# Kernel tuning notes

Measured on AMD Instinct MI355X. Metric: run time of the kernel, lower is better.

Reference implementation:

```python
import jax, jax.numpy as jnp
import numpy as np


def _conv1x1(t, W, b):
    # 1x1 conv == per-pixel channel GEMM: [B,C,H,W] x [O,C] -> [B,O,H,W]
    return jnp.einsum('bchw,oc->bohw', t, W) + b[None, :, None, None]


def setup_inputs() -> dict:
    key = jax.random.key(0)
    ks = jax.random.split(key, 10)
    B, C, H, W = 8, 256, 96, 96
    s = 1.0 / np.sqrt(C)
    inp = {
        'x': jax.random.normal(ks[0], (B, C, H, W), dtype=jnp.float32),
        'Wq': jax.random.normal(ks[1], (C, C), dtype=jnp.float32) * s,
        'bq': jax.random.normal(ks[2], (C,), dtype=jnp.float32) * 0.01,
        'Wk': jax.random.normal(ks[3], (C, C), dtype=jnp.float32) * s,
        'bk': jax.random.normal(ks[4], (C,), dtype=jnp.float32) * 0.01,
        'Wv': jax.random.normal(ks[5], (C, C), dtype=jnp.float32) * s,
        'bv': jax.random.normal(ks[6], (C,), dtype=jnp.float32) * 0.01,
        'Ws': jax.random.normal(ks[7], (C, C), dtype=jnp.float32) * s,
        'bs': jax.random.normal(ks[8], (C,), dtype=jnp.float32) * 0.01,
        # torch init is zeros; use a nonzero scalar so the attention branch matters
        'gamma': jax.random.normal(ks[9], (1,), dtype=jnp.float32) * 0.5,
    }
    return inp


def reference(x, Wq, bq, Wk, bk, Wv, bv, Ws, bs, gamma):
    B, C, H, W = x.shape
    N = H * W
    # query: [B, N, C]
    q = _conv1x1(x, Wq, bq).reshape(B, C, N).transpose(0, 2, 1)
    # key: 1x1 conv, then stride-3 1x1 conv (== subsample every 3rd pixel, then GEMM)
    k = _conv1x1(x, Wk, bk)
    k = _conv1x1(k[:, :, ::3, ::3], Ws, bs)
    Ns = k.shape[2] * k.shape[3]
    k = k.reshape(B, C, Ns)
    energy = jnp.einsum('bnc,bcm->bnm', q, k)       # [B, N, Ns]
    attn = jax.nn.softmax(energy, axis=-1)
    # value: same 1x1 conv + strided 1x1 conv pipeline
    v = _conv1x1(x, Wv, bv)
    v = _conv1x1(v[:, :, ::3, ::3], Ws, bs).reshape(B, C, Ns)
    out = jnp.einsum('bcm,bnm->bcn', v, attn).reshape(B, C, H, W)
    return gamma[0] * out + x
```

## Files before the change

kernel.cpp:

```cpp
#include <hip/hip_runtime.h>

typedef _Float16 f16;
typedef _Float16 f16x8 __attribute__((ext_vector_type(8)));
typedef __fp16 fp16x2 __attribute__((ext_vector_type(2)));
typedef float f32x4 __attribute__((ext_vector_type(4)));
typedef float f32x16 __attribute__((ext_vector_type(16)));

#define CDIM 256
#define NPIX 9216
#define NB 8

__device__ __forceinline__ f32x4 mfma16(f16x8 a, f16x8 b, f32x4 c) {
  return __builtin_amdgcn_mfma_f32_16x16x32_f16(a, b, c, 0, 0, 0);
}
__device__ __forceinline__ f32x16 mfma32(f16x8 a, f16x8 b, f32x16 c) {
  return __builtin_amdgcn_mfma_f32_32x32x16_f16(a, b, c, 0, 0, 0);
}
__device__ __forceinline__ f16x8 ld8(const f16* p) { return *(const f16x8*)p; }

__device__ __forceinline__ void stage16(const void* g, void* l) {
  __builtin_amdgcn_global_load_lds((const __attribute__((address_space(1))) unsigned int*)g,
                                   (__attribute__((address_space(3))) unsigned int*)l, 16, 0, 0);
}
#define S_BARRIER() do { asm volatile("" ::: "memory"); __builtin_amdgcn_s_barrier(); asm volatile("" ::: "memory"); } while (0)
#define WAIT_VM(N) do { asm volatile("s_waitcnt vmcnt(" #N ")" ::: "memory"); __builtin_amdgcn_sched_barrier(0); } while (0)

__device__ __forceinline__ unsigned pkrtz(float a, float b) {
  union { fp16x2 h; unsigned u; } cv;
  cv.h = __builtin_amdgcn_cvt_pkrtz(a, b);
  return cv.u;
}
union U8 { f16x8 v; unsigned u[4]; };

__device__ __forceinline__ f16x8 pack_swap(float v0, float v1, float v2, float v3,
                                           float v4, float v5, float v6, float v7,
                                           int hh) {
  unsigned a  = pkrtz(v0, v1);
  unsigned b2 = pkrtz(v2, v3);
  unsigned c2 = pkrtz(v4, v5);
  unsigned d2 = pkrtz(v6, v7);
  unsigned ex1 = __shfl_xor(hh ? a : c2, 32);
  unsigned ex2 = __shfl_xor(hh ? b2 : d2, 32);
  U8 r;
  r.u[0] = hh ? ex1 : a;
  r.u[1] = hh ? ex2 : b2;
  r.u[2] = hh ? c2 : ex1;
  r.u[3] = hh ? d2 : ex2;
  return r.v;
}


__global__ void prep_weights(const float* __restrict__ Wq,
                             const float* __restrict__ Wk, const float* __restrict__ bk,
                             const float* __restrict__ Wv, const float* __restrict__ bv,
                             const float* __restrict__ Ws, const float* __restrict__ bs,
                             f16* __restrict__ WqF, f16* __restrict__ Wk2H, f16* __restrict__ Wv2H,
                             float* __restrict__ bk2, float* __restrict__ bv2) {
  int o = blockIdx.x, c = threadIdx.x;
  float ak = 0.f, av = 0.f;
  for (int i = 0; i < CDIM; ++i) {
    float w = Ws[o*CDIM + i];
    ak += w * Wk[i*CDIM + c];
    av += w * Wv[i*CDIM + c];
  }
  Wk2H[o*CDIM + c] = (f16)ak;
  Wv2H[o*CDIM + c] = (f16)av;
  {
    size_t byte = (size_t)((o >> 5)*16 + (c >> 4))*1024
                + (size_t)(((c >> 3) & 1)*32 + (o & 31))*16 + (c & 7)*2;
    *(f16*)((char*)WqF + byte) = (f16)Wq[o*CDIM + c];
  }
  if (c == 0) {
    float sk = 0.f, sv = 0.f;
    for (int i = 0; i < CDIM; ++i) { float w = Ws[o*CDIM + i]; sk += w*bk[i]; sv += w*bv[i]; }
    bk2[o] = sk + bs[o];
    bv2[o] = sv + bs[o];
  }
}

__global__ void transpose_x(const float* __restrict__ x, char* __restrict__ xT) {
  __shared__ f16 tile[32][34];
  int c0 = blockIdx.x * 32, n0 = blockIdx.y * 32, b = blockIdx.z;
  int tx = threadIdx.x, ty = threadIdx.y;
#pragma unroll
  for (int j = 0; j < 4; ++j) {
    int cl = ty + 8*j;
    tile[cl][tx] = (f16)x[(size_t)(b*CDIM + c0 + cl)*NPIX + n0 + tx];
  }
  __syncthreads();
  int tid = ty*32 + tx;
  if (tid < 128) {
    int nl = tid >> 2, u = tid & 3;
    int n = n0 + nl;
    int cu = (c0 >> 3) + u;
    f16x8 v;
#pragma unroll
    for (int e = 0; e < 8; ++e) v[e] = tile[8*u + e][nl];
    size_t byte = (size_t)(b*NPIX + n)*512 + (size_t)((cu ^ (n & 7)) << 4);
    *(f16x8*)(xT + byte) = v;
  }
}

__global__ __launch_bounds__(256) void compute_kv(
    const char* __restrict__ xT, const f16* __restrict__ Wk2H, const f16* __restrict__ Wv2H,
    const float* __restrict__ bk2, const float* __restrict__ bv2,
    char* __restrict__ kB, char* __restrict__ vB) {
  int ch = blockIdx.x;
  int m0 = ch * 32;
  int b = blockIdx.y;
  int tid = threadIdx.x;
  int w = tid >> 6, lane = tid & 63, l15 = lane & 15, q = lane >> 4;
  size_t chbase = (size_t)(b*32 + ch)*16384;

  const char* xrow[2]; int xn7[2];
#pragma unroll
  for (int mt2 = 0; mt2 < 2; ++mt2) {
    int m = m0 + 16*mt2 + l15;
    int n = 288*(m >> 5) + 3*(m & 31);
    xrow[mt2] = xT + (size_t)(b*NPIX + n)*512;
    xn7[mt2] = n & 7;
  }
  const f16 *kwb[4], *vwb[4];
#pragma unroll
  for (int t = 0; t < 4; ++t) {
    kwb[t] = Wk2H + (size_t)(64*w + 16*t + l15)*CDIM + 8*q;
    vwb[t] = Wv2H + (size_t)(64*w + 16*t + l15)*CDIM + 8*q;
  }
  f32x4 accK[2][4] = {};
  f32x4 accV[4][2] = {};
  for (int ks = 0; ks < 8; ++ks) {
    f16x8 am[2], wk[4], wv[4];
#pragma unroll
    for (int mt2 = 0; mt2 < 2; ++mt2)
      am[mt2] = *(const f16x8*)(xrow[mt2] + (((q + 4*ks) ^ xn7[mt2]) << 4));
#pragma unroll
    for (int t = 0; t < 4; ++t) { wk[t] = ld8(kwb[t] + 32*ks); wv[t] = ld8(vwb[t] + 32*ks); }
#pragma unroll
    for (int mt2 = 0; mt2 < 2; ++mt2)
#pragma unroll
      for (int ot = 0; ot < 4; ++ot) {
        accK[mt2][ot] = mfma16(am[mt2], wk[ot], accK[mt2][ot]);
        accV[ot][mt2] = mfma16(wv[ot], am[mt2], accV[ot][mt2]);
      }
  }
#pragma unroll
  for (int mt2 = 0; mt2 < 2; ++mt2)
#pragma unroll
    for (int ot = 0; ot < 4; ++ot) {
      int cin = 64*w + 16*ot + l15;
      float bo = bk2[cin];
      size_t fb = chbase + (size_t)(cin >> 4)*1024 + (size_t)(((cin >> 3) & 1)*32)*16 + (cin & 7)*2;
#pragma unroll
      for (int r = 0; r < 4; ++r) {
        int keyrel = 16*mt2 + 4*q + r;
        *(f16*)(kB + fb + (size_t)keyrel*16) = (f16)(accK[mt2][ot][r] + bo);
      }
    }
#pragma unroll
  for (int ct = 0; ct < 4; ++ct) {
    f32x4 bv4 = *(const f32x4*)(bv2 + 64*w + 16*ct + 4*q);
#pragma unroll
    for (int mt2 = 0; mt2 < 2; ++mt2) {
#pragma unroll
      for (int r = 0; r < 4; ++r) {
        int c = 64*w + 16*ct + 4*q + r;
        size_t byte = chbase + (size_t)(2*(c >> 5) + mt2)*1024
                    + (size_t)((l15 >> 3)*32 + (c & 31))*16 + (l15 & 7)*2;
        *(f16*)(vB + byte) = (f16)(accV[ct][mt2][r] + bv4[r]);
      }
    }
  }
}

__global__ __launch_bounds__(256, 2) void attention(
    const char* __restrict__ xT, const f16* __restrict__ WqF, const float* __restrict__ bq,
    const char* __restrict__ kB, const char* __restrict__ vB,
    const float* __restrict__ xg, const float* __restrict__ gamma_p,
    float* __restrict__ out) {
  __shared__ char lds[65536];

  int bid = blockIdx.x;
  int b = bid & 7;
  int tile = bid >> 3;
  int tid = threadIdx.x;
  int w = tid >> 6, lane = tid & 63, l31 = lane & 31, hh = lane >> 5;
  int n0w = tile*128 + w*32;
  int lane16 = lane * 16;

  const char* kBb = kB + (size_t)b*524288;
  const char* vBb = vB + (size_t)b*524288;

  {
    int so = tid * 16;
#pragma unroll
    for (int r = 0; r < 4; ++r) stage16(kBb + so + r*4096, lds + so + r*4096);
#pragma unroll
    for (int r = 0; r < 4; ++r) stage16(vBb + so + r*4096, lds + 16384 + so + r*4096);
  }

  f16x8 qf[16];
  {
    f16x8 xb[16];
    int n = n0w + l31;
    const char* xrow = xT + (size_t)(b*NPIX + n)*512;
    int n7 = n & 7;
#pragma unroll
    for (int s = 0; s < 16; ++s)
      xb[s] = *(const f16x8*)(xrow + (((2*s + hh) ^ n7) << 4));
#pragma unroll
    for (int ot = 0; ot < 8; ++ot) {
      f32x16 acc;
#pragma unroll
      for (int j = 0; j < 16; ++j) acc[j] = 0.f;
#pragma unroll
      for (int s = 0; s < 16; ++s) {
        f16x8 wa = *(const f16x8*)((const char*)WqF + (size_t)(ot*16 + s)*1024 + lane16);
        acc = mfma32(wa, xb[s], acc);
      }
#pragma unroll
      for (int i = 0; i < 4; ++i) {
        f32x4 bv4 = *(const f32x4*)(bq + 32*ot + 8*i + 4*hh);
#pragma unroll
        for (int j2 = 0; j2 < 4; ++j2) acc[4*i + j2] += bv4[j2];
      }
      qf[2*ot + 0] = pack_swap(acc[0], acc[1], acc[2], acc[3],
                               acc[4], acc[5], acc[6], acc[7], hh);
      qf[2*ot + 1] = pack_swap(acc[8], acc[9], acc[10], acc[11],
                               acc[12], acc[13], acc[14], acc[15], hh);
    }
  }

  f32x16 O[8];
#pragma unroll
  for (int i = 0; i < 8; ++i)
#pragma unroll
    for (int j = 0; j < 16; ++j) O[i][j] = 0.f;
  float m_run = -3e38f, l_run = 0.f;

  for (int t = 0; t < 32; ++t) {
    char* curb = lds + ((t & 1) << 15);
    if (t < 31) {
      const char* ksrc = kBb + (size_t)(t + 1)*16384;
      const char* vsrc = vBb + (size_t)(t + 1)*16384;
      char* kd = lds + (((t + 1) & 1) << 15);
      int so = tid * 16;
#pragma unroll
      for (int r = 0; r < 4; ++r) stage16(ksrc + so + r*4096, kd + so + r*4096);
#pragma unroll
      for (int r = 0; r < 4; ++r) stage16(vsrc + so + r*4096, kd + 16384 + so + r*4096);
      WAIT_VM(8);
    } else {
      WAIT_VM(0);
    }
    S_BARRIER();

    f32x16 S16;
#pragma unroll
    for (int j = 0; j < 16; ++j) S16[j] = 0.f;
    __builtin_amdgcn_s_setprio(1);
#pragma unroll
    for (int s = 0; s < 16; ++s) {
      f16x8 kf = *(const f16x8*)(curb + s*1024 + lane16);
      S16 = mfma32(kf, qf[s], S16);
    }
    __builtin_amdgcn_s_setprio(0);

    float mx = S16[0];
#pragma unroll
    for (int j = 1; j < 16; ++j) mx = fmaxf(mx, S16[j]);
    mx = fmaxf(mx, __shfl_xor(mx, 32));
    if (!__all(mx <= m_run + 8.0f)) {
      float mn = fmaxf(m_run, mx);
      float al = __expf(m_run - mn);
      m_run = mn;
      l_run *= al;
#pragma unroll
      for (int i = 0; i < 8; ++i)
#pragma unroll
        for (int j = 0; j < 16; ++j) O[i][j] *= al;
    }
    float p[16];
    float ls = 0.f;
#pragma unroll
    for (int j = 0; j < 16; ++j) { p[j] = __expf(S16[j] - m_run); ls += p[j]; }
    l_run += ls;

    f16x8 pf0 = pack_swap(p[0], p[1], p[2], p[3], p[4], p[5], p[6], p[7], hh);
    f16x8 pf1 = pack_swap(p[8], p[9], p[10], p[11], p[12], p[13], p[14], p[15], hh);

    __builtin_amdgcn_s_setprio(1);
#pragma unroll
    for (int ct = 0; ct < 8; ++ct) {
      f16x8 vf0 = *(const f16x8*)(curb + 16384 + (ct*2 + 0)*1024 + lane16);
      O[ct] = mfma32(vf0, pf0, O[ct]);
      f16x8 vf1 = *(const f16x8*)(curb + 16384 + (ct*2 + 1)*1024 + lane16);
      O[ct] = mfma32(vf1, pf1, O[ct]);
    }
    __builtin_amdgcn_s_setprio(0);
    S_BARRIER();
  }

  l_run += __shfl_xor(l_run, 32);
  float inv = 1.0f / l_run;
  float g = gamma_p[0];
  int n = n0w + l31;
#pragma unroll
  for (int ct = 0; ct < 8; ++ct)
#pragma unroll
    for (int j = 0; j < 16; ++j) {
      int c = 32*ct + (j & 3) + 8*(j >> 2) + 4*hh;
      size_t idx = (size_t)(b*CDIM + c)*NPIX + n;
      out[idx] = g * (O[ct][j] * inv) + xg[idx];
    }
}

extern "C" void kernel_launch(void* const* d_in, const int* in_sizes, int n_in,
                              void* d_out, int out_size, void* d_ws, size_t ws_size,
                              hipStream_t stream) {
  (void)in_sizes; (void)n_in; (void)out_size; (void)ws_size;
  const float* x     = (const float*)d_in[0];
  const float* Wq    = (const float*)d_in[1];
  const float* bq    = (const float*)d_in[2];
  const float* Wk    = (const float*)d_in[3];
  const float* bk    = (const float*)d_in[4];
  const float* Wv    = (const float*)d_in[5];
  const float* bv    = (const float*)d_in[6];
  const float* Ws    = (const float*)d_in[7];
  const float* bs    = (const float*)d_in[8];
  const float* gamma = (const float*)d_in[9];

  char* ws = (char*)d_ws;
  float* bk2 = (float*)(ws);
  float* bv2 = (float*)(ws + 1024);
  char* xT   = ws + 4096;
  char* kB   = ws + 4096 + 37748736;
  char* vB   = kB + 4194304;
  f16* WqF   = (f16*)(vB + 4194304);
  f16* Wk2H  = WqF + 65536;
  f16* Wv2H  = Wk2H + 65536;

  prep_weights<<<256, 256, 0, stream>>>(Wq, Wk, bk, Wv, bv, Ws, bs, WqF, Wk2H, Wv2H, bk2, bv2);
  transpose_x<<<dim3(8, 288, 8), dim3(32, 8), 0, stream>>>(x, xT);
  compute_kv<<<dim3(32, 8), 256, 0, stream>>>(xT, Wk2H, Wv2H, bk2, bv2, kB, vB);
  attention<<<576, 256, 0, stream>>>(xT, WqF, bq, kB, vB, x, gamma, (float*)d_out);
}
```

Before: 197.2 us.

## Split attention output channels across two wave groups with 512-thread blocks

The attention kernel now runs 8 waves per block. Each pair of waves shares the same 32 query rows and computes the full QK^T and softmax redundantly, but each wave owns only half of the 256 output channels in the PV product. This halves the O accumulator registers per wave and spreads the K/V staging loads over twice as many threads. The QK^T chain is also split into two independent accumulators to shorten the MFMA dependency chain. The cost is that QK^T, the Q projection and the exp work are duplicated in both waves of a pair.

```diff
diff --git a/kernel.cpp b/kernel.cpp
--- a/kernel.cpp
+++ b/kernel.cpp
@@ -172,7 +172,7 @@
   }
 }
 
-__global__ __launch_bounds__(256, 2) void attention(
+__global__ __launch_bounds__(512, 2) void attention(
     const char* __restrict__ xT, const f16* __restrict__ WqF, const float* __restrict__ bq,
     const char* __restrict__ kB, const char* __restrict__ vB,
     const float* __restrict__ xg, const float* __restrict__ gamma_p,
@@ -184,7 +184,8 @@
   int tile = bid >> 3;
   int tid = threadIdx.x;
   int w = tid >> 6, lane = tid & 63, l31 = lane & 31, hh = lane >> 5;
-  int n0w = tile*128 + w*32;
+  int rt = w & 3, cs = w >> 2;
+  int n0w = tile*128 + rt*32;
   int lane16 = lane * 16;
 
   const char* kBb = kB + (size_t)b*524288;
@@ -192,10 +193,10 @@
 
   {
     int so = tid * 16;
-#pragma unroll
-    for (int r = 0; r < 4; ++r) stage16(kBb + so + r*4096, lds + so + r*4096);
-#pragma unroll
-    for (int r = 0; r < 4; ++r) stage16(vBb + so + r*4096, lds + 16384 + so + r*4096);
+    stage16(kBb + so, lds + so);
+    stage16(kBb + so + 8192, lds + so + 8192);
+    stage16(vBb + so, lds + 16384 + so);
+    stage16(vBb + so + 8192, lds + 16384 + so + 8192);
   }
 
   f16x8 qf[16];
@@ -230,9 +231,9 @@
     }
   }
 
-  f32x16 O[8];
-#pragma unroll
-  for (int i = 0; i < 8; ++i)
+  f32x16 O[4];
+#pragma unroll
+  for (int i = 0; i < 4; ++i)
 #pragma unroll
     for (int j = 0; j < 16; ++j) O[i][j] = 0.f;
   float m_run = -3e38f, l_run = 0.f;
@@ -244,26 +245,31 @@
       const char* vsrc = vBb + (size_t)(t + 1)*16384;
       char* kd = lds + (((t + 1) & 1) << 15);
       int so = tid * 16;
-#pragma unroll
-      for (int r = 0; r < 4; ++r) stage16(ksrc + so + r*4096, kd + so + r*4096);
-#pragma unroll
-      for (int r = 0; r < 4; ++r) stage16(vsrc + so + r*4096, kd + 16384 + so + r*4096);
-      WAIT_VM(8);
+      stage16(ksrc + so, kd + so);
+      stage16(ksrc + so + 8192, kd + so + 8192);
+      stage16(vsrc + so, kd + 16384 + so);
+      stage16(vsrc + so + 8192, kd + 16384 + so + 8192);
+      WAIT_VM(4);
     } else {
       WAIT_VM(0);
     }
     S_BARRIER();
 
+    f32x16 Sa, Sb;
+#pragma unroll
+    for (int j = 0; j < 16; ++j) { Sa[j] = 0.f; Sb[j] = 0.f; }
+    __builtin_amdgcn_s_setprio(1);
+#pragma unroll
+    for (int s = 0; s < 8; ++s) {
+      f16x8 kfa = *(const f16x8*)(curb + (2*s)*1024 + lane16);
+      Sa = mfma32(kfa, qf[2*s], Sa);
+      f16x8 kfb = *(const f16x8*)(curb + (2*s + 1)*1024 + lane16);
+      Sb = mfma32(kfb, qf[2*s + 1], Sb);
+    }
+    __builtin_amdgcn_s_setprio(0);
     f32x16 S16;
 #pragma unroll
-    for (int j = 0; j < 16; ++j) S16[j] = 0.f;
-    __builtin_amdgcn_s_setprio(1);
-#pragma unroll
-    for (int s = 0; s < 16; ++s) {
-      f16x8 kf = *(const f16x8*)(curb + s*1024 + lane16);
-      S16 = mfma32(kf, qf[s], S16);
-    }
-    __builtin_amdgcn_s_setprio(0);
+    for (int j = 0; j < 16; ++j) S16[j] = Sa[j] + Sb[j];
 
     float mx = S16[0];
 #pragma unroll
@@ -275,7 +281,7 @@
       m_run = mn;
       l_run *= al;
 #pragma unroll
-      for (int i = 0; i < 8; ++i)
+      for (int i = 0; i < 4; ++i)
 #pragma unroll
         for (int j = 0; j < 16; ++j) O[i][j] *= al;
     }
@@ -290,10 +296,11 @@
 
     __builtin_amdgcn_s_setprio(1);
 #pragma unroll
-    for (int ct = 0; ct < 8; ++ct) {
-      f16x8 vf0 = *(const f16x8*)(curb + 16384 + (ct*2 + 0)*1024 + lane16);
+    for (int ct = 0; ct < 4; ++ct) {
+      int ctg = cs*4 + ct;
+      f16x8 vf0 = *(const f16x8*)(curb + 16384 + (ctg*2 + 0)*1024 + lane16);
       O[ct] = mfma32(vf0, pf0, O[ct]);
-      f16x8 vf1 = *(const f16x8*)(curb + 16384 + (ct*2 + 1)*1024 + lane16);
+      f16x8 vf1 = *(const f16x8*)(curb + 16384 + (ctg*2 + 1)*1024 + lane16);
       O[ct] = mfma32(vf1, pf1, O[ct]);
     }
     __builtin_amdgcn_s_setprio(0);
@@ -305,10 +312,10 @@
   float g = gamma_p[0];
   int n = n0w + l31;
 #pragma unroll
-  for (int ct = 0; ct < 8; ++ct)
+  for (int ct = 0; ct < 4; ++ct)
 #pragma unroll
     for (int j = 0; j < 16; ++j) {
-      int c = 32*ct + (j & 3) + 8*(j >> 2) + 4*hh;
+      int c = 32*(cs*4 + ct) + (j & 3) + 8*(j >> 2) + 4*hh;
       size_t idx = (size_t)(b*CDIM + c)*NPIX + n;
       out[idx] = g * (O[ct][j] * inv) + xg[idx];
     }
@@ -342,5 +349,5 @@
   prep_weights<<<256, 256, 0, stream>>>(Wq, Wk, bk, Wv, bv, Ws, bs, WqF, Wk2H, Wv2H, bk2, bv2);
   transpose_x<<<dim3(8, 288, 8), dim3(32, 8), 0, stream>>>(x, xT);
   compute_kv<<<dim3(32, 8), 256, 0, stream>>>(xT, Wk2H, Wv2H, bk2, bv2, kB, vB);
-  attention<<<576, 256, 0, stream>>>(xT, WqF, bq, kB, vB, x, gamma, (float*)d_out);
-}
+  attention<<<576, 512, 0, stream>>>(xT, WqF, bq, kB, vB, x, gamma, (float*)d_out);
+}
```

After: 269.6 us. 1.37x slower.

## Software-pipeline QK^T one tile ahead with triple-buffered K/V in LDS

Applied to the files above, without the earlier changes.

The attention loop now computes the next tile's QK^T scores while running softmax and PV on the current tile, using two ping-pong score accumulators. K is prefetched two tiles ahead and V one tile ahead into triple-buffered LDS regions (96KB), and the trailing per-iteration barrier and setprio hints are removed. The goal is to overlap exp and softmax VALU work with MFMA and to hide load latency. In exchange, the larger LDS footprint and extra registers drop occupancy from 2 to 1 block per CU.

```diff
diff --git a/kernel.cpp b/kernel.cpp
--- a/kernel.cpp
+++ b/kernel.cpp
@@ -172,12 +172,12 @@
   }
 }
 
-__global__ __launch_bounds__(256, 2) void attention(
+__global__ __launch_bounds__(256, 1) void attention(
     const char* __restrict__ xT, const f16* __restrict__ WqF, const float* __restrict__ bq,
     const char* __restrict__ kB, const char* __restrict__ vB,
     const float* __restrict__ xg, const float* __restrict__ gamma_p,
     float* __restrict__ out) {
-  __shared__ char lds[65536];
+  __shared__ char lds[98304];
 
   int bid = blockIdx.x;
   int b = bid & 7;
@@ -189,13 +189,16 @@
 
   const char* kBb = kB + (size_t)b*524288;
   const char* vBb = vB + (size_t)b*524288;
+  char* vbase = lds + 49152;
 
   {
     int so = tid * 16;
 #pragma unroll
     for (int r = 0; r < 4; ++r) stage16(kBb + so + r*4096, lds + so + r*4096);
 #pragma unroll
-    for (int r = 0; r < 4; ++r) stage16(vBb + so + r*4096, lds + 16384 + so + r*4096);
+    for (int r = 0; r < 4; ++r) stage16(vBb + so + r*4096, vbase + so + r*4096);
+#pragma unroll
+    for (int r = 0; r < 4; ++r) stage16(kBb + 16384 + so + r*4096, lds + 16384 + so + r*4096);
   }
 
   f16x8 qf[16];
@@ -229,6 +232,8 @@
                                acc[12], acc[13], acc[14], acc[15], hh);
     }
   }
+  WAIT_VM(0);
+  S_BARRIER();
 
   f32x16 O[8];
 #pragma unroll
@@ -236,38 +241,48 @@
 #pragma unroll
     for (int j = 0; j < 16; ++j) O[i][j] = 0.f;
   float m_run = -3e38f, l_run = 0.f;
-
-  for (int t = 0; t < 32; ++t) {
-    char* curb = lds + ((t & 1) << 15);
+  float g = gamma_p[0];
+
+  f32x16 SA, SB;
+#pragma unroll
+  for (int j = 0; j < 16; ++j) SA[j] = 0.f;
+#pragma unroll
+  for (int s = 0; s < 16; ++s) {
+    f16x8 kf = *(const f16x8*)(lds + s*1024 + lane16);
+    SA = mfma32(kf, qf[s], SA);
+  }
+
+  auto body = [&](f32x16& Scur, f32x16& Snext, int t) {
+    int so = tid * 16;
+    if (t + 2 < 32) {
+      const char* ksrc = kBb + (size_t)(t + 2)*16384;
+      char* kd = lds + ((t + 2) % 3)*16384;
+#pragma unroll
+      for (int r = 0; r < 4; ++r) stage16(ksrc + so + r*4096, kd + so + r*4096);
+    }
+    if (t + 1 < 32) {
+      const char* vsrc = vBb + (size_t)(t + 1)*16384;
+      char* vd = vbase + ((t + 1) % 3)*16384;
+#pragma unroll
+      for (int r = 0; r < 4; ++r) stage16(vsrc + so + r*4096, vd + so + r*4096);
+    }
+    if (t < 30) { WAIT_VM(8); } else if (t == 30) { WAIT_VM(4); } else { WAIT_VM(0); }
+    S_BARRIER();
+
     if (t < 31) {
-      const char* ksrc = kBb + (size_t)(t + 1)*16384;
-      const char* vsrc = vBb + (size_t)(t + 1)*16384;
-      char* kd = lds + (((t + 1) & 1) << 15);
-      int so = tid * 16;
-#pragma unroll
-      for (int r = 0; r < 4; ++r) stage16(ksrc + so + r*4096, kd + so + r*4096);
-#pragma unroll
-      for (int r = 0; r < 4; ++r) stage16(vsrc + so + r*4096, kd + 16384 + so + r*4096);
-      WAIT_VM(8);
-    } else {
-      WAIT_VM(0);
-    }
-    S_BARRIER();
-
-    f32x16 S16;
-#pragma unroll
-    for (int j = 0; j < 16; ++j) S16[j] = 0.f;
-    __builtin_amdgcn_s_setprio(1);
-#pragma unroll
-    for (int s = 0; s < 16; ++s) {
-      f16x8 kf = *(const f16x8*)(curb + s*1024 + lane16);
-      S16 = mfma32(kf, qf[s], S16);
-    }
-    __builtin_amdgcn_s_setprio(0);
-
-    float mx = S16[0];
-#pragma unroll
-    for (int j = 1; j < 16; ++j) mx = fmaxf(mx, S16[j]);
+      const char* kc = lds + ((t + 1) % 3)*16384;
+#pragma unroll
+      for (int j = 0; j < 16; ++j) Snext[j] = 0.f;
+#pragma unroll
+      for (int s = 0; s < 16; ++s) {
+        f16x8 kf = *(const f16x8*)(kc + s*1024 + lane16);
+        Snext = mfma32(kf, qf[s], Snext);
+      }
+    }
+
+    float mx = Scur[0];
+#pragma unroll
+    for (int j = 1; j < 16; ++j) mx = fmaxf(mx, Scur[j]);
     mx = fmaxf(mx, __shfl_xor(mx, 32));
     if (!__all(mx <= m_run + 8.0f)) {
       float mn = fmaxf(m_run, mx);
@@ -279,30 +294,34 @@
 #pragma unroll
         for (int j = 0; j < 16; ++j) O[i][j] *= al;
     }
-    float p[16];
     float ls = 0.f;
 #pragma unroll
-    for (int j = 0; j < 16; ++j) { p[j] = __expf(S16[j] - m_run); ls += p[j]; }
+    for (int j = 0; j < 16; ++j) { Scur[j] = __expf(Scur[j] - m_run); ls += Scur[j]; }
     l_run += ls;
 
-    f16x8 pf0 = pack_swap(p[0], p[1], p[2], p[3], p[4], p[5], p[6], p[7], hh);
-    f16x8 pf1 = pack_swap(p[8], p[9], p[10], p[11], p[12], p[13], p[14], p[15], hh);
-
-    __builtin_amdgcn_s_setprio(1);
+    f16x8 pf0 = pack_swap(Scur[0], Scur[1], Scur[2], Scur[3],
+                          Scur[4], Scur[5], Scur[6], Scur[7], hh);
+    f16x8 pf1 = pack_swap(Scur[8], Scur[9], Scur[10], Scur[11],
+                          Scur[12], Scur[13], Scur[14], Scur[15], hh);
+
+    const char* vc = vbase + (t % 3)*16384;
 #pragma unroll
     for (int ct = 0; ct < 8; ++ct) {
-      f16x8 vf0 = *(const f16x8*)(curb + 16384 + (ct*2 + 0)*1024 + lane16);
+      f16x8 vf0 = *(const f16x8*)(vc + (ct*2 + 0)*1024 + lane16);
       O[ct] = mfma32(vf0, pf0, O[ct]);
-      f16x8 vf1 = *(const f16x8*)(curb + 16384 + (ct*2 + 1)*1024 + lane16);
+      f16x8 vf1 = *(const f16x8*)(vc + (ct*2 + 1)*1024 + lane16);
       O[ct] = mfma32(vf1, pf1, O[ct]);
     }
-    __builtin_amdgcn_s_setprio(0);
-    S_BARRIER();
+  };
+
+#pragma unroll 1
+  for (int tp = 0; tp < 32; tp += 2) {
+    body(SA, SB, tp);
+    body(SB, SA, tp + 1);
   }
 
   l_run += __shfl_xor(l_run, 32);
   float inv = 1.0f / l_run;
-  float g = gamma_p[0];
   int n = n0w + l31;
 #pragma unroll
   for (int ct = 0; ct < 8; ++ct)
```

Result: slower. 267.4 us (+35.6%).

## Switch attention to 16x16x32 MFMA tiles with smaller query tiles and more blocks

Applied to the files above, without the earlier changes.

The attention kernel moves from 32x32x16 to 16x16x32 MFMA, so each wave now handles 16 query pixels instead of 32. The block count doubles to 1152, and the K, V and Wq fragment layouts written by prep_weights and compute_kv are redone so operands line up without the cross-half shuffle packing. The intent is fewer registers per wave, no shfl-based pack_swap, and better occupancy and grid fill across CUs. In exchange each K/V tile staged into LDS is reused by half as many queries, which doubles K/V global and LDS traffic per output.

```diff
diff --git a/kernel.cpp b/kernel.cpp
--- a/kernel.cpp
+++ b/kernel.cpp
@@ -4,7 +4,6 @@
 typedef _Float16 f16x8 __attribute__((ext_vector_type(8)));
 typedef __fp16 fp16x2 __attribute__((ext_vector_type(2)));
 typedef float f32x4 __attribute__((ext_vector_type(4)));
-typedef float f32x16 __attribute__((ext_vector_type(16)));
 
 #define CDIM 256
 #define NPIX 9216
@@ -12,9 +11,6 @@
 
 __device__ __forceinline__ f32x4 mfma16(f16x8 a, f16x8 b, f32x4 c) {
   return __builtin_amdgcn_mfma_f32_16x16x32_f16(a, b, c, 0, 0, 0);
-}
-__device__ __forceinline__ f32x16 mfma32(f16x8 a, f16x8 b, f32x16 c) {
-  return __builtin_amdgcn_mfma_f32_32x32x16_f16(a, b, c, 0, 0, 0);
 }
 __device__ __forceinline__ f16x8 ld8(const f16* p) { return *(const f16x8*)p; }
 
@@ -31,22 +27,8 @@
   return cv.u;
 }
 union U8 { f16x8 v; unsigned u[4]; };
-
-__device__ __forceinline__ f16x8 pack_swap(float v0, float v1, float v2, float v3,
-                                           float v4, float v5, float v6, float v7,
-                                           int hh) {
-  unsigned a  = pkrtz(v0, v1);
-  unsigned b2 = pkrtz(v2, v3);
-  unsigned c2 = pkrtz(v4, v5);
-  unsigned d2 = pkrtz(v6, v7);
-  unsigned ex1 = __shfl_xor(hh ? a : c2, 32);
-  unsigned ex2 = __shfl_xor(hh ? b2 : d2, 32);
-  U8 r;
-  r.u[0] = hh ? ex1 : a;
-  r.u[1] = hh ? ex2 : b2;
-  r.u[2] = hh ? c2 : ex1;
-  r.u[3] = hh ? d2 : ex2;
-  return r.v;
+__device__ __forceinline__ f16x8 mk8(unsigned a, unsigned b, unsigned c, unsigned d) {
+  U8 r; r.u[0] = a; r.u[1] = b; r.u[2] = c; r.u[3] = d; return r.v;
 }
 
 
@@ -66,8 +48,9 @@
   Wk2H[o*CDIM + c] = (f16)ak;
   Wv2H[o*CDIM + c] = (f16)av;
   {
-    size_t byte = (size_t)((o >> 5)*16 + (c >> 4))*1024
-                + (size_t)(((c >> 3) & 1)*32 + (o & 31))*16 + (c & 7)*2;
+    int og = o >> 4, sp = c >> 5;
+    int lane = 16*((c >> 3) & 3) + (o & 15);
+    size_t byte = (size_t)(og*8 + sp)*1024 + (size_t)lane*16 + (c & 7)*2;
     *(f16*)((char*)WqF + byte) = (f16)Wq[o*CDIM + c];
   }
   if (c == 0) {
@@ -149,11 +132,14 @@
     for (int ot = 0; ot < 4; ++ot) {
       int cin = 64*w + 16*ot + l15;
       float bo = bk2[cin];
-      size_t fb = chbase + (size_t)(cin >> 4)*1024 + (size_t)(((cin >> 3) & 1)*32)*16 + (cin & 7)*2;
+      int f = 2*(cin >> 5) + mt2;
+      int q_s = (cin >> 2) & 3;
+      int e_s = 4*((cin >> 4) & 1) + (cin & 3);
+      size_t fb = chbase + (size_t)f*1024 + (size_t)(16*q_s)*16 + e_s*2;
 #pragma unroll
       for (int r = 0; r < 4; ++r) {
-        int keyrel = 16*mt2 + 4*q + r;
-        *(f16*)(kB + fb + (size_t)keyrel*16) = (f16)(accK[mt2][ot][r] + bo);
+        int krel15 = 4*q + r;
+        *(f16*)(kB + fb + (size_t)krel15*16) = (f16)(accK[mt2][ot][r] + bo);
       }
     }
 #pragma unroll
@@ -161,11 +147,13 @@
     f32x4 bv4 = *(const f32x4*)(bv2 + 64*w + 16*ct + 4*q);
 #pragma unroll
     for (int mt2 = 0; mt2 < 2; ++mt2) {
+      int q_s = (l15 >> 2) & 3;
+      int e_s = 4*mt2 + (l15 & 3);
 #pragma unroll
       for (int r = 0; r < 4; ++r) {
         int c = 64*w + 16*ct + 4*q + r;
-        size_t byte = chbase + (size_t)(2*(c >> 5) + mt2)*1024
-                    + (size_t)((l15 >> 3)*32 + (c & 31))*16 + (l15 & 7)*2;
+        size_t byte = chbase + (size_t)(c >> 4)*1024
+                    + (size_t)(16*q_s + (c & 15))*16 + e_s*2;
         *(f16*)(vB + byte) = (f16)(accV[ct][mt2][r] + bv4[r]);
       }
     }
@@ -183,8 +171,8 @@
   int b = bid & 7;
   int tile = bid >> 3;
   int tid = threadIdx.x;
-  int w = tid >> 6, lane = tid & 63, l31 = lane & 31, hh = lane >> 5;
-  int n0w = tile*128 + w*32;
+  int w = tid >> 6, lane = tid & 63, l15 = lane & 15, q = lane >> 4;
+  int n0w = tile*64 + w*16;
   int lane16 = lane * 16;
 
   const char* kBb = kB + (size_t)b*524288;
@@ -198,43 +186,40 @@
     for (int r = 0; r < 4; ++r) stage16(vBb + so + r*4096, lds + 16384 + so + r*4096);
   }
 
-  f16x8 qf[16];
+  f16x8 qf[8];
   {
-    f16x8 xb[16];
-    int n = n0w + l31;
+    f16x8 xb[8];
+    int n = n0w + l15;
     const char* xrow = xT + (size_t)(b*NPIX + n)*512;
     int n7 = n & 7;
 #pragma unroll
-    for (int s = 0; s < 16; ++s)
-      xb[s] = *(const f16x8*)(xrow + (((2*s + hh) ^ n7) << 4));
-#pragma unroll
-    for (int ot = 0; ot < 8; ++ot) {
-      f32x16 acc;
-#pragma unroll
-      for (int j = 0; j < 16; ++j) acc[j] = 0.f;
-#pragma unroll
-      for (int s = 0; s < 16; ++s) {
-        f16x8 wa = *(const f16x8*)((const char*)WqF + (size_t)(ot*16 + s)*1024 + lane16);
-        acc = mfma32(wa, xb[s], acc);
+    for (int sp = 0; sp < 8; ++sp)
+      xb[sp] = *(const f16x8*)(xrow + (((4*sp + q) ^ n7) << 4));
+    f32x4 qacc[16];
+#pragma unroll
+    for (int og = 0; og < 16; ++og) {
+      f32x4 acc = {0.f, 0.f, 0.f, 0.f};
+#pragma unroll
+      for (int sp = 0; sp < 8; ++sp) {
+        f16x8 wa = *(const f16x8*)((const char*)WqF + (size_t)(og*8 + sp)*1024 + lane16);
+        acc = mfma16(wa, xb[sp], acc);
       }
-#pragma unroll
-      for (int i = 0; i < 4; ++i) {
-        f32x4 bv4 = *(const f32x4*)(bq + 32*ot + 8*i + 4*hh);
-#pragma unroll
-        for (int j2 = 0; j2 < 4; ++j2) acc[4*i + j2] += bv4[j2];
-      }
-      qf[2*ot + 0] = pack_swap(acc[0], acc[1], acc[2], acc[3],
-                               acc[4], acc[5], acc[6], acc[7], hh);
-      qf[2*ot + 1] = pack_swap(acc[8], acc[9], acc[10], acc[11],
-                               acc[12], acc[13], acc[14], acc[15], hh);
-    }
-  }
-
-  f32x16 O[8];
-#pragma unroll
-  for (int i = 0; i < 8; ++i)
-#pragma unroll
-    for (int j = 0; j < 16; ++j) O[i][j] = 0.f;
+      f32x4 bq4 = *(const f32x4*)(bq + og*16 + 4*q);
+#pragma unroll
+      for (int r = 0; r < 4; ++r) acc[r] += bq4[r];
+      qacc[og] = acc;
+    }
+#pragma unroll
+    for (int s = 0; s < 8; ++s)
+      qf[s] = mk8(pkrtz(qacc[2*s][0],   qacc[2*s][1]),
+                  pkrtz(qacc[2*s][2],   qacc[2*s][3]),
+                  pkrtz(qacc[2*s+1][0], qacc[2*s+1][1]),
+                  pkrtz(qacc[2*s+1][2], qacc[2*s+1][3]));
+  }
+
+  f32x4 O[16];
+#pragma unroll
+  for (int i = 0; i < 16; ++i) O[i] = (f32x4){0.f, 0.f, 0.f, 0.f};
   float m_run = -3e38f, l_run = 0.f;
 
   for (int t = 0; t < 32; ++t) {
@@ -254,20 +239,20 @@
     }
     S_BARRIER();
 
-    f32x16 S16;
-#pragma unroll
-    for (int j = 0; j < 16; ++j) S16[j] = 0.f;
+    f32x4 S0 = {0.f, 0.f, 0.f, 0.f}, S1 = {0.f, 0.f, 0.f, 0.f};
     __builtin_amdgcn_s_setprio(1);
 #pragma unroll
-    for (int s = 0; s < 16; ++s) {
-      f16x8 kf = *(const f16x8*)(curb + s*1024 + lane16);
-      S16 = mfma32(kf, qf[s], S16);
+    for (int s = 0; s < 8; ++s) {
+      f16x8 kf0 = *(const f16x8*)(curb + (2*s)*1024 + lane16);
+      S0 = mfma16(kf0, qf[s], S0);
+      f16x8 kf1 = *(const f16x8*)(curb + (2*s + 1)*1024 + lane16);
+      S1 = mfma16(kf1, qf[s], S1);
     }
     __builtin_amdgcn_s_setprio(0);
 
-    float mx = S16[0];
-#pragma unroll
-    for (int j = 1; j < 16; ++j) mx = fmaxf(mx, S16[j]);
+    float mx = fmaxf(fmaxf(fmaxf(S0[0], S0[1]), fmaxf(S0[2], S0[3])),
+                     fmaxf(fmaxf(S1[0], S1[1]), fmaxf(S1[2], S1[3])));
+    mx = fmaxf(mx, __shfl_xor(mx, 16));
     mx = fmaxf(mx, __shfl_xor(mx, 32));
     if (!__all(mx <= m_run + 8.0f)) {
       float mn = fmaxf(m_run, mx);
@@ -275,42 +260,42 @@
       m_run = mn;
       l_run *= al;
 #pragma unroll
-      for (int i = 0; i < 8; ++i)
-#pragma unroll
-        for (int j = 0; j < 16; ++j) O[i][j] *= al;
-    }
-    float p[16];
+      for (int i = 0; i < 16; ++i)
+#pragma unroll
+        for (int r = 0; r < 4; ++r) O[i][r] *= al;
+    }
     float ls = 0.f;
 #pragma unroll
-    for (int j = 0; j < 16; ++j) { p[j] = __expf(S16[j] - m_run); ls += p[j]; }
+    for (int r = 0; r < 4; ++r) { S0[r] = __expf(S0[r] - m_run); ls += S0[r]; }
+#pragma unroll
+    for (int r = 0; r < 4; ++r) { S1[r] = __expf(S1[r] - m_run); ls += S1[r]; }
     l_run += ls;
 
-    f16x8 pf0 = pack_swap(p[0], p[1], p[2], p[3], p[4], p[5], p[6], p[7], hh);
-    f16x8 pf1 = pack_swap(p[8], p[9], p[10], p[11], p[12], p[13], p[14], p[15], hh);
+    f16x8 pf = mk8(pkrtz(S0[0], S0[1]), pkrtz(S0[2], S0[3]),
+                   pkrtz(S1[0], S1[1]), pkrtz(S1[2], S1[3]));
 
     __builtin_amdgcn_s_setprio(1);
 #pragma unroll
-    for (int ct = 0; ct < 8; ++ct) {
-      f16x8 vf0 = *(const f16x8*)(curb + 16384 + (ct*2 + 0)*1024 + lane16);
-      O[ct] = mfma32(vf0, pf0, O[ct]);
-      f16x8 vf1 = *(const f16x8*)(curb + 16384 + (ct*2 + 1)*1024 + lane16);
-      O[ct] = mfma32(vf1, pf1, O[ct]);
+    for (int cg = 0; cg < 16; ++cg) {
+      f16x8 vf = *(const f16x8*)(curb + 16384 + cg*1024 + lane16);
+      O[cg] = mfma16(vf, pf, O[cg]);
     }
     __builtin_amdgcn_s_setprio(0);
     S_BARRIER();
   }
 
+  l_run += __shfl_xor(l_run, 16);
   l_run += __shfl_xor(l_run, 32);
   float inv = 1.0f / l_run;
   float g = gamma_p[0];
-  int n = n0w + l31;
-#pragma unroll
-  for (int ct = 0; ct < 8; ++ct)
-#pragma unroll
-    for (int j = 0; j < 16; ++j) {
-      int c = 32*ct + (j & 3) + 8*(j >> 2) + 4*hh;
+  int n = n0w + l15;
+#pragma unroll
+  for (int cg = 0; cg < 16; ++cg)
+#pragma unroll
+    for (int r = 0; r < 4; ++r) {
+      int c = 16*cg + 4*q + r;
       size_t idx = (size_t)(b*CDIM + c)*NPIX + n;
-      out[idx] = g * (O[ct][j] * inv) + xg[idx];
+      out[idx] = g * (O[cg][r] * inv) + xg[idx];
     }
 }
 
@@ -342,5 +327,5 @@
   prep_weights<<<256, 256, 0, stream>>>(Wq, Wk, bk, Wv, bv, Ws, bs, WqF, Wk2H, Wv2H, bk2, bv2);
   transpose_x<<<dim3(8, 288, 8), dim3(32, 8), 0, stream>>>(x, xT);
   compute_kv<<<dim3(32, 8), 256, 0, stream>>>(xT, Wk2H, Wv2H, bk2, bv2, kB, vB);
-  attention<<<576, 256, 0, stream>>>(xT, WqF, bq, kB, vB, x, gamma, (float*)d_out);
-}
+  attention<<<1152, 256, 0, stream>>>(xT, WqF, bq, kB, vB, x, gamma, (float*)d_out);
+}
```

Result: slower. 206.3 us (+4.6%).
